# Kernel tuning notes

Hardware: AMD Instinct MI355X
Metric: run time of the kernel (lower is better)

Reference implementation:

```python
import jax, jax.numpy as jnp
import numpy as np
from jax import lax

# Config mirrors TemporalLePEAttention(dim=256, resolution=(56,56), idx=0, split_size=4, num_heads=8, temporal=True)
B, T, H, W, C = 2, 2, 56, 56, 256
NH = 8
HD = C // NH
SS = 4                      # split_size
H_sp, W_sp = H, SS          # idx == 0 -> strip windows of full height
nWh, nWw = H // H_sp, W // W_sp   # 1, 14
SCALE = HD ** -0.5
KH, KW = W_sp, H_sp         # unfold kernel = focal_window = [W_sp, H_sp] = (4, 56)
PH, PW = 0, H_sp // 2       # idx == 0 padding = [0, H_sp//2]
NW = B * nWh * nWw          # number of windows
TQ = T * H_sp * W_sp        # query tokens per window


def setup_inputs() -> dict:
    key = jax.random.key(0)
    k1, k2 = jax.random.split(key, 2)
    qkv = jax.random.normal(k1, (3, B, T, H, W, C), jnp.float32)
    # depthwise 3x3 LePE conv (nn.Conv2d(dim, dim, 3, padding=1, groups=dim))
    get_v_w = jax.random.normal(k2, (C, 1, 3, 3), jnp.float32) * 0.1
    get_v_b = jnp.zeros((C,), jnp.float32)
    # pool linear initialized as in the module: weight = SS/(H_sp*W_sp), bias = 0
    pool_w = jnp.full((SS, H_sp * W_sp), SS / (H_sp * W_sp), jnp.float32)
    pool_b = jnp.zeros((SS,), jnp.float32)
    return {"qkv": qkv, "get_v_w": get_v_w, "get_v_b": get_v_b,
            "pool_w": pool_w, "pool_b": pool_b}


def _windows_thw(x):
    # im2ddca_temporal: (B,T,H,W,C) -> (B*nWh*nWw, NH, T*H_sp*W_sp, HD)
    x = x.reshape(B, T, nWh, H_sp, nWw, W_sp, C).transpose(0, 2, 4, 1, 3, 5, 6)
    x = x.reshape(NW, TQ, NH, HD).transpose(0, 2, 1, 3)
    return x


def _lepe_temporal(v, w, b):
    # get_lepe_temporal: window v, depthwise 3x3 conv, return (v_win, lepe) as (NW, NH, TQ, HD)
    xw = v.reshape(B, T, nWh, H_sp, nWw, W_sp, C).transpose(0, 2, 4, 1, 6, 3, 5)
    xw = xw.reshape(-1, C, H_sp, W_sp)  # (B*nWh*nWw*T, C, H_sp, W_sp)
    lepe = lax.conv_general_dilated(xw, w, (1, 1), 'SAME', feature_group_count=C,
                                    dimension_numbers=('NCHW', 'OIHW', 'NCHW'))
    lepe = lepe + b[None, :, None, None]

    def fmt(t):
        t = t.reshape(NW, T, NH, HD, H_sp * W_sp).transpose(0, 2, 1, 4, 3)
        return t.reshape(NW, NH, TQ, HD)
    return fmt(xw), fmt(lepe)


def _pool_unfold(t, pool_w, pool_b):
    # focal pooling: per-window linear over H_sp*W_sp -> SS, then unfold over pooled map
    tw = t.reshape(B, T, nWh, H_sp, nWw, W_sp, C).transpose(0, 2, 4, 1, 6, 3, 5)
    tw = tw.reshape(B, nWh, nWw, T, C, H_sp * W_sp)
    p = jnp.einsum('bhwtcn,sn->bhwtcs', tw, pool_w) + pool_b  # (B,nWh,nWw,T,C,SS)
    # flatten(-2) + permute + reshape -> pooled map (B*T, C, SS*nWh, nWw)  (idx == 0)
    pm = p.transpose(0, 3, 4, 5, 1, 2).reshape(B * T, C, SS * nWh, nWw)
    # nn.Unfold(kernel=(KH,KW), padding=(PH,PW), stride=1); here out_h == 1
    pmp = jnp.pad(pm, ((0, 0), (0, 0), (PH, PH), (PW, PW)))
    ow = pmp.shape[3] - KW + 1  # = nWw + 1
    patches = jnp.stack([pmp[:, :, :, i:i + KW] for i in range(ow)], axis=1)  # (BT, ow, C, KH, KW)
    u = patches.reshape(B, T, ow, C, KH, KW).transpose(0, 2, 1, 4, 5, 3)      # (B, ow, T, KH, KW, C)
    u = u.reshape(B * ow, T * KH * KW, NH, HD).transpose(0, 2, 1, 3)          # (B*ow, NH, Tkk, HD)
    # idx == 0: view (B, nWh, -1, ...) and drop the last unfold location -> one per window
    u = u.reshape(B, nWh, ow // nWh, NH, T * KH * KW, HD)[:, :, :-1]
    return u.reshape(NW, NH, T * KH * KW, HD)


def reference(qkv, get_v_w, get_v_b, pool_w, pool_b):
    q_in, k_in, v_in = qkv[0], qkv[1], qkv[2]
    q = _windows_thw(q_in) * SCALE                      # (NW, NH, TQ, HD)
    k = _windows_thw(k_in)
    v, lepe = _lepe_temporal(v_in, get_v_w, get_v_b)
    kp = _pool_unfold(k_in, pool_w, pool_b)             # (NW, NH, TQ, HD)
    vp = _pool_unfold(v_in, pool_w, pool_b)
    k = jnp.concatenate([k, kp], axis=2)                # (NW, NH, 2*TQ, HD)
    v = jnp.concatenate([v, vp], axis=2)
    attn = jax.nn.softmax(jnp.einsum('wnqd,wnkd->wnqk', q, k), axis=-1)
    x = jnp.einsum('wnqk,wnkd->wnqd', attn, v) + lepe   # (NW, NH, TQ, HD)
    x = x.transpose(0, 2, 1, 3).reshape(NW, TQ, C)
    # windows2img_temporal -> (B, T, H, W, C)
    x = x.reshape(B, nWh, nWw, T, H_sp, W_sp, C).transpose(0, 3, 1, 4, 2, 5, 6)
    return x.reshape(B, T, H, W, C)
```

## Files before the change

### kernel.cpp

```cpp
#include <hip/hip_runtime.h>
#include <hip/hip_bf16.h>

#define B_   2
#define T_   2
#define H_   56
#define W_   56
#define C_   256
#define NH_  8
#define HD_  32
#define NWW_ 14
#define TQ_  448
#define SEQ_ 576
#define REAL_ 560
#define VIRT_ 320.0f
#define MEXP_ 16.0f
#define PMSTR_ 57344

typedef __bf16 bf16;
typedef __bf16 bf16x8 __attribute__((ext_vector_type(8)));
typedef __bf16 bf16x4 __attribute__((ext_vector_type(4)));
typedef float  f32x4  __attribute__((ext_vector_type(4)));
typedef short  s16x4  __attribute__((ext_vector_type(4)));
typedef unsigned int  uint;
typedef uint   uint4v __attribute__((ext_vector_type(4)));
typedef uint   uint2v __attribute__((ext_vector_type(2)));
typedef unsigned short u16;

#if defined(__has_builtin)
#  if __has_builtin(__builtin_amdgcn_mfma_f32_16x16x16bf16_1k)
#    define USE_MFMA16 1
#  endif
#endif
#ifndef USE_MFMA16
#  define USE_MFMA16 0
#endif

__device__ __forceinline__ uint pack2(float a, float b) {
    u16 ha = __builtin_bit_cast(u16, (bf16)a);
    u16 hb = __builtin_bit_cast(u16, (bf16)b);
    return (uint)ha | ((uint)hb << 16);
}

__global__ void pre_kernel(const float* __restrict__ k_in, const float* __restrict__ v_in,
                           const float* __restrict__ pool_w, const float* __restrict__ pool_b,
                           const float* __restrict__ gw, const float* __restrict__ gb,
                           float* __restrict__ pmk_part, float* __restrict__ pmv_part,
                           bf16* __restrict__ lepe) {
    __shared__ float pws[4][56];
    const int bid = blockIdx.x;
    const int c   = threadIdx.x;

    if (bid < 224) {
        const int quarter = bid & 3;
        const int bj = bid >> 2;
        const int j  = bj % NWW_;
        const int t  = (bj / NWW_) % T_;
        const int b  = bj / (NWW_ * T_);
        const int n0 = quarter * 56;

        if (c < 224) pws[c / 56][c % 56] = pool_w[(c / 56) * 224 + n0 + (c % 56)];
        __syncthreads();

        float ak[4], av[4];
        #pragma unroll
        for (int s = 0; s < 4; ++s) {
            ak[s] = (quarter == 0) ? pool_b[s] : 0.f;
            av[s] = 0.f;
        }
        for (int i = 0; i < 56; ++i) {
            const int n = n0 + i;
            const int h = n >> 2, wi = n & 3;
            const size_t off = ((size_t)(((b * T_ + t) * H_ + h) * W_ + (j * 4 + wi))) * C_ + c;
            const float kv = k_in[off];
            const float vv = v_in[off];
            #pragma unroll
            for (int s = 0; s < 4; ++s) {
                ak[s] += kv * pws[s][i];
                av[s] += vv * pws[s][i];
            }
        }
        #pragma unroll
        for (int s = 0; s < 4; ++s) {
            const size_t o = (size_t)quarter * PMSTR_ +
                             ((size_t)(((b * T_ + t) * 4 + s) * NWW_ + j)) * C_ + c;
            pmk_part[o] = ak[s];
            pmv_part[o] = av[s];
        }
    } else {
        const int r  = bid - 224;
        const int sp = r % 7;
        const int h  = (r / 7) % H_;
        const int bt = r / (7 * H_);

        float wv9[9];
        #pragma unroll
        for (int k = 0; k < 9; ++k) wv9[k] = gw[c * 9 + k];
        const float bias = gb[c];

        #pragma unroll
        for (int s2 = 0; s2 < 2; ++s2) {
            const int strip = sp * 2 + s2;
            float tile[3][4];
            #pragma unroll
            for (int dy = 0; dy < 3; ++dy) {
                const int hh = h - 1 + dy;
                const bool ok = (hh >= 0 && hh < H_);
                #pragma unroll
                for (int x = 0; x < 4; ++x) {
                    tile[dy][x] = ok
                        ? v_in[((size_t)(bt * H_ + hh) * W_ + (strip * 4 + x)) * C_ + c]
                        : 0.f;
                }
            }
            #pragma unroll
            for (int wi = 0; wi < 4; ++wi) {
                float acc = bias;
                #pragma unroll
                for (int dy = 0; dy < 3; ++dy) {
                    #pragma unroll
                    for (int dx = -1; dx <= 1; ++dx) {
                        const int xx = wi + dx;
                        if (xx >= 0 && xx < 4)
                            acc += wv9[dy * 3 + dx + 1] * tile[dy][xx];
                    }
                }
                lepe[((size_t)(bt * H_ + h) * W_ + (strip * 4 + wi)) * C_ + c] = (bf16)acc;
            }
        }
    }
}

__launch_bounds__(896, 4)
__global__ void attn_kernel(const float* __restrict__ q_in, const float* __restrict__ k_in,
                            const float* __restrict__ v_in, const float* __restrict__ pm_k,
                            const float* __restrict__ pm_v, const bf16* __restrict__ lepe,
                            float* __restrict__ out) {
    __shared__ __align__(16) u16 Ks[SEQ_ * 40];
    __shared__ __align__(16) u16 Vt[32 * 584];

    const int tid  = threadIdx.x;
    const int nh   = blockIdx.x & 7;
    const int nwi  = blockIdx.x >> 3;
    const int b    = nwi / NWW_;
    const int ww   = nwi % NWW_;
    const int cbase = nh * 32;

    for (int idx = tid; idx < SEQ_ * 4; idx += 896) {
        const int tok = idx >> 2, slot = idx & 3;
        uint4v dk = {0, 0, 0, 0}, dv = {0, 0, 0, 0};
        if (tok < TQ_) {
            const int t = tok / 224, r = tok % 224;
            const int h = r >> 2, wi = r & 3;
            const size_t off =
                ((size_t)(((b * T_ + t) * H_ + h) * W_ + (ww * 4 + wi))) * C_ + cbase + slot * 8;
            const f32x4 k0 = *(const f32x4*)(k_in + off);
            const f32x4 k1 = *(const f32x4*)(k_in + off + 4);
            const f32x4 v0 = *(const f32x4*)(v_in + off);
            const f32x4 v1 = *(const f32x4*)(v_in + off + 4);
            dk = uint4v{pack2(k0[0], k0[1]), pack2(k0[2], k0[3]),
                        pack2(k1[0], k1[1]), pack2(k1[2], k1[3])};
            dv = uint4v{pack2(v0[0], v0[1]), pack2(v0[2], v0[3]),
                        pack2(v1[0], v1[1]), pack2(v1[2], v1[3])};
        } else if (tok < REAL_) {
            const int i = tok - TQ_;
            const int t = i / 56, r = i % 56;
            const int kh = r / 14, jj = r % 14;
            const size_t off =
                ((size_t)(((b * T_ + t) * 4 + kh) * NWW_ + jj)) * C_ + cbase + slot * 8;
            f32x4 k0 = {0,0,0,0}, k1 = {0,0,0,0}, v0 = {0,0,0,0}, v1 = {0,0,0,0};
            #pragma unroll
            for (int pq = 0; pq < 4; ++pq) {
                const float* pk = pm_k + (size_t)pq * PMSTR_ + off;
                const float* pv = pm_v + (size_t)pq * PMSTR_ + off;
                k0 += *(const f32x4*)pk;  k1 += *(const f32x4*)(pk + 4);
                v0 += *(const f32x4*)pv;  v1 += *(const f32x4*)(pv + 4);
            }
            dk = uint4v{pack2(k0[0], k0[1]), pack2(k0[2], k0[3]),
                        pack2(k1[0], k1[1]), pack2(k1[2], k1[3])};
            dv = uint4v{pack2(v0[0], v0[1]), pack2(v0[2], v0[3]),
                        pack2(v1[0], v1[1]), pack2(v1[2], v1[3])};
        }
        *(uint4v*)(Ks + tok * 40 + slot * 8) = dk;
        u16 es[8];
        #pragma unroll
        for (int e = 0; e < 8; ++e) es[e] = (u16)((dv[e >> 1] >> ((e & 1) * 16)) & 0xffff);
        #pragma unroll
        for (int e = 0; e < 8; ++e) Vt[(slot * 8 + e) * 584 + tok] = es[e];
    }
    __syncthreads();

    const int lane = tid & 63;
    const int wv   = tid >> 6;
    const int l15  = lane & 15;
    const int g    = lane >> 4;
    const float QS = 0.17677669529663687f * 1.4426950408889634f;

    bf16x8 qf[2];
    #pragma unroll
    for (int ti = 0; ti < 2; ++ti) {
        const int qrow = (wv + ti * 14) * 16 + l15;
        const int t = qrow / 224, r = qrow % 224;
        const int h = r >> 2, wi = r & 3;
        const size_t off =
            ((size_t)(((b * T_ + t) * H_ + h) * W_ + (ww * 4 + wi))) * C_ + cbase + g * 8;
        const f32x4 a0 = *(const f32x4*)(q_in + off);
        const f32x4 a1 = *(const f32x4*)(q_in + off + 4);
        const uint4v qp = {pack2(a0[0] * QS, a0[1] * QS), pack2(a0[2] * QS, a0[3] * QS),
                           pack2(a1[0] * QS, a1[1] * QS), pack2(a1[2] * QS, a1[3] * QS)};
        qf[ti] = __builtin_bit_cast(bf16x8, qp);
    }

    f32x4 o[2][2];
    float ssum[2];
    const f32x4 zf = {0.f, 0.f, 0.f, 0.f};
    #pragma unroll
    for (int ti = 0; ti < 2; ++ti) {
        o[ti][0] = zf; o[ti][1] = zf; ssum[ti] = 0.f;
    }

    for (int kc = 0; kc < SEQ_ / 32; ++kc) {
        const int kt0 = kc * 32;
        const bf16x8 ka = *(const bf16x8*)(Ks + (kt0 + l15) * 40 + g * 8);
        const bf16x8 kb = *(const bf16x8*)(Ks + (kt0 + 16 + l15) * 40 + g * 8);
#if USE_MFMA16
        const s16x4 va00 = __builtin_bit_cast(s16x4, *(const uint2v*)(Vt + l15 * 584 + kt0 + g * 4));
        const s16x4 va01 = __builtin_bit_cast(s16x4, *(const uint2v*)(Vt + l15 * 584 + kt0 + 16 + g * 4));
        const s16x4 va10 = __builtin_bit_cast(s16x4, *(const uint2v*)(Vt + (16 + l15) * 584 + kt0 + g * 4));
        const s16x4 va11 = __builtin_bit_cast(s16x4, *(const uint2v*)(Vt + (16 + l15) * 584 + kt0 + 16 + g * 4));
#else
        const bf16x8 va = *(const bf16x8*)(Vt + l15 * 584 + kt0 + g * 8);
        const bf16x8 vb = *(const bf16x8*)(Vt + (16 + l15) * 584 + kt0 + g * 8);
#endif

        #pragma unroll
        for (int ti = 0; ti < 2; ++ti) {
            const f32x4 s0 = __builtin_amdgcn_mfma_f32_16x16x32_bf16(ka, qf[ti], zf, 0, 0, 0);
            const f32x4 s1 = __builtin_amdgcn_mfma_f32_16x16x32_bf16(kb, qf[ti], zf, 0, 0, 0);

            const float p0 = __builtin_amdgcn_exp2f(s0[0] - MEXP_);
            const float p1 = __builtin_amdgcn_exp2f(s0[1] - MEXP_);
            const float p2 = __builtin_amdgcn_exp2f(s0[2] - MEXP_);
            const float p3 = __builtin_amdgcn_exp2f(s0[3] - MEXP_);
            const float p4 = __builtin_amdgcn_exp2f(s1[0] - MEXP_);
            const float p5 = __builtin_amdgcn_exp2f(s1[1] - MEXP_);
            const float p6 = __builtin_amdgcn_exp2f(s1[2] - MEXP_);
            const float p7 = __builtin_amdgcn_exp2f(s1[3] - MEXP_);

            ssum[ti] += ((p0 + p1) + (p2 + p3)) + ((p4 + p5) + (p6 + p7));

            const uint w0 = pack2(p0, p1), w1 = pack2(p2, p3);
            const uint w2 = pack2(p4, p5), w3 = pack2(p6, p7);
#if USE_MFMA16
            const s16x4 pb0 = __builtin_bit_cast(s16x4, uint2v{w0, w1});
            const s16x4 pb1 = __builtin_bit_cast(s16x4, uint2v{w2, w3});
            o[ti][0] = __builtin_amdgcn_mfma_f32_16x16x16bf16_1k(va00, pb0, o[ti][0], 0, 0, 0);
            o[ti][0] = __builtin_amdgcn_mfma_f32_16x16x16bf16_1k(va01, pb1, o[ti][0], 0, 0, 0);
            o[ti][1] = __builtin_amdgcn_mfma_f32_16x16x16bf16_1k(va10, pb0, o[ti][1], 0, 0, 0);
            o[ti][1] = __builtin_amdgcn_mfma_f32_16x16x16bf16_1k(va11, pb1, o[ti][1], 0, 0, 0);
#else
            const int baseln = l15 + ((g & 1) << 5);
            const uint sA = (g & 2) ? w2 : w0;
            const uint sB = (g & 2) ? w3 : w1;
            const uint o0 = (uint)__shfl((int)sA, baseln);
            const uint o1 = (uint)__shfl((int)sB, baseln);
            const uint o2 = (uint)__shfl((int)sA, baseln + 16);
            const uint o3 = (uint)__shfl((int)sB, baseln + 16);
            const bf16x8 pf = __builtin_bit_cast(bf16x8, uint4v{o0, o1, o2, o3});
            o[ti][0] = __builtin_amdgcn_mfma_f32_16x16x32_bf16(pf, va, o[ti][0], 0, 0, 0);
            o[ti][1] = __builtin_amdgcn_mfma_f32_16x16x32_bf16(pf, vb, o[ti][1], 0, 0, 0);
#endif
        }
    }

    #pragma unroll
    for (int ti = 0; ti < 2; ++ti) {
        float den = ssum[ti];
        den += __shfl_xor(den, 16);
        den += __shfl_xor(den, 32);
        den += VIRT_ * 0.0000152587890625f;
        const float osc = 1.0f / den;

#if USE_MFMA16
        const int qrow = (wv + ti * 14) * 16 + l15;
        const int t = qrow / 224, rr = qrow % 224;
        const int h = rr >> 2, wi = rr & 3;
        const size_t off =
            ((size_t)(((b * T_ + t) * H_ + h) * W_ + (ww * 4 + wi))) * C_ + cbase;
        #pragma unroll
        for (int h2 = 0; h2 < 2; ++h2) {
            const int co = h2 * 16 + g * 4;
            const bf16x4 lp = *(const bf16x4*)(lepe + off + co);
            f32x4 val;
            #pragma unroll
            for (int r = 0; r < 4; ++r) val[r] = o[ti][h2][r] * osc + (float)lp[r];
            *(f32x4*)(out + off + co) = val;
        }
#else
        #pragma unroll
        for (int r = 0; r < 4; ++r) {
            const float oscr = __shfl(osc, g * 4 + r);
            const int qrow = (wv + ti * 14) * 16 + g * 4 + r;
            const int t = qrow / 224, rr = qrow % 224;
            const int h = rr >> 2, wi = rr & 3;
            const size_t off =
                ((size_t)(((b * T_ + t) * H_ + h) * W_ + (ww * 4 + wi))) * C_ + cbase + l15;
            out[off]      = o[ti][0][r] * oscr + (float)lepe[off];
            out[off + 16] = o[ti][1][r] * oscr + (float)lepe[off + 16];
        }
#endif
    }
}

extern "C" void kernel_launch(void* const* d_in, const int* in_sizes, int n_in,
                              void* d_out, int out_size, void* d_ws, size_t ws_size,
                              hipStream_t stream) {
    const float* qkv = (const float*)d_in[0];
    const float* gw  = (const float*)d_in[1];
    const float* gb  = (const float*)d_in[2];
    const float* pw  = (const float*)d_in[3];
    const float* pb  = (const float*)d_in[4];

    const size_t plane = (size_t)B_ * T_ * H_ * W_ * C_;
    const float* q_in = qkv;
    const float* k_in = qkv + plane;
    const float* v_in = qkv + 2 * plane;

    float* pmk_part = (float*)d_ws;
    float* pmv_part = pmk_part + 4 * PMSTR_;
    bf16*  lepe     = (bf16*)(pmv_part + 4 * PMSTR_);
    float* outp     = (float*)d_out;

    hipLaunchKernelGGL(pre_kernel, dim3(224 + 1568), dim3(256), 0, stream,
                       k_in, v_in, pw, pb, gw, gb, pmk_part, pmv_part, lepe);
    hipLaunchKernelGGL(attn_kernel, dim3(28 * 8), dim3(896), 0, stream,
                       q_in, k_in, v_in, pmk_part, pmv_part, lepe, outp);
}
```

Baseline: 44.51 us.

## Split attention blocks across query halves, pad K rows to 36, prefetch K/V fragments

```diff
diff --git a/kernel.cpp b/kernel.cpp
--- a/kernel.cpp
+++ b/kernel.cpp
@@ -15,6 +15,7 @@
 #define VIRT_ 320.0f
 #define MEXP_ 16.0f
 #define PMSTR_ 57344
+#define KSTR_ 36
 
 typedef __bf16 bf16;
 typedef __bf16 bf16x8 __attribute__((ext_vector_type(8)));
@@ -39,6 +40,13 @@
     u16 ha = __builtin_bit_cast(u16, (bf16)a);
     u16 hb = __builtin_bit_cast(u16, (bf16)b);
     return (uint)ha | ((uint)hb << 16);
+}
+
+__device__ __forceinline__ bf16x8 ldK(const u16* p) {
+    const uint2v a = *(const uint2v*)p;
+    const uint2v b = *(const uint2v*)(p + 4);
+    const uint4v u = {a[0], a[1], b[0], b[1]};
+    return __builtin_bit_cast(bf16x8, u);
 }
 
 __global__ void pre_kernel(const float* __restrict__ k_in, const float* __restrict__ v_in,
@@ -130,22 +138,24 @@
     }
 }
 
-__launch_bounds__(896, 4)
+__launch_bounds__(448, 4)
 __global__ void attn_kernel(const float* __restrict__ q_in, const float* __restrict__ k_in,
                             const float* __restrict__ v_in, const float* __restrict__ pm_k,
                             const float* __restrict__ pm_v, const bf16* __restrict__ lepe,
                             float* __restrict__ out) {
-    __shared__ __align__(16) u16 Ks[SEQ_ * 40];
+    __shared__ __align__(16) u16 Ks[SEQ_ * KSTR_];
     __shared__ __align__(16) u16 Vt[32 * 584];
 
     const int tid  = threadIdx.x;
-    const int nh   = blockIdx.x & 7;
-    const int nwi  = blockIdx.x >> 3;
+    const int bid  = blockIdx.x;
+    const int half = bid & 1;
+    const int nh   = (bid >> 1) & 7;
+    const int nwi  = bid >> 4;
     const int b    = nwi / NWW_;
     const int ww   = nwi % NWW_;
     const int cbase = nh * 32;
 
-    for (int idx = tid; idx < SEQ_ * 4; idx += 896) {
+    for (int idx = tid; idx < SEQ_ * 4; idx += 448) {
         const int tok = idx >> 2, slot = idx & 3;
         uint4v dk = {0, 0, 0, 0}, dv = {0, 0, 0, 0};
         if (tok < TQ_) {
@@ -180,7 +190,8 @@
             dv = uint4v{pack2(v0[0], v0[1]), pack2(v0[2], v0[3]),
                         pack2(v1[0], v1[1]), pack2(v1[2], v1[3])};
         }
-        *(uint4v*)(Ks + tok * 40 + slot * 8) = dk;
+        *(uint2v*)(Ks + tok * KSTR_ + slot * 8)     = uint2v{dk[0], dk[1]};
+        *(uint2v*)(Ks + tok * KSTR_ + slot * 8 + 4) = uint2v{dk[2], dk[3]};
         u16 es[8];
         #pragma unroll
         for (int e = 0; e < 8; ++e) es[e] = (u16)((dv[e >> 1] >> ((e & 1) * 16)) & 0xffff);
@@ -195,10 +206,11 @@
     const int g    = lane >> 4;
     const float QS = 0.17677669529663687f * 1.4426950408889634f;
 
+    const int tbase = half * 14 + wv;
     bf16x8 qf[2];
     #pragma unroll
     for (int ti = 0; ti < 2; ++ti) {
-        const int qrow = (wv + ti * 14) * 16 + l15;
+        const int qrow = (tbase + ti * 7) * 16 + l15;
         const int t = qrow / 224, r = qrow % 224;
         const int h = r >> 2, wi = r & 3;
         const size_t off =
@@ -218,24 +230,13 @@
         o[ti][0] = zf; o[ti][1] = zf; ssum[ti] = 0.f;
     }
 
-    for (int kc = 0; kc < SEQ_ / 32; ++kc) {
-        const int kt0 = kc * 32;
-        const bf16x8 ka = *(const bf16x8*)(Ks + (kt0 + l15) * 40 + g * 8);
-        const bf16x8 kb = *(const bf16x8*)(Ks + (kt0 + 16 + l15) * 40 + g * 8);
 #if USE_MFMA16
-        const s16x4 va00 = __builtin_bit_cast(s16x4, *(const uint2v*)(Vt + l15 * 584 + kt0 + g * 4));
-        const s16x4 va01 = __builtin_bit_cast(s16x4, *(const uint2v*)(Vt + l15 * 584 + kt0 + 16 + g * 4));
-        const s16x4 va10 = __builtin_bit_cast(s16x4, *(const uint2v*)(Vt + (16 + l15) * 584 + kt0 + g * 4));
-        const s16x4 va11 = __builtin_bit_cast(s16x4, *(const uint2v*)(Vt + (16 + l15) * 584 + kt0 + 16 + g * 4));
-#else
-        const bf16x8 va = *(const bf16x8*)(Vt + l15 * 584 + kt0 + g * 8);
-        const bf16x8 vb = *(const bf16x8*)(Vt + (16 + l15) * 584 + kt0 + g * 8);
-#endif
-
+    auto compute = [&](const bf16x8& KA, const bf16x8& KB, const s16x4& V00,
+                       const s16x4& V01, const s16x4& V10, const s16x4& V11) {
         #pragma unroll
         for (int ti = 0; ti < 2; ++ti) {
-            const f32x4 s0 = __builtin_amdgcn_mfma_f32_16x16x32_bf16(ka, qf[ti], zf, 0, 0, 0);
-            const f32x4 s1 = __builtin_amdgcn_mfma_f32_16x16x32_bf16(kb, qf[ti], zf, 0, 0, 0);
+            const f32x4 s0 = __builtin_amdgcn_mfma_f32_16x16x32_bf16(KA, qf[ti], zf, 0, 0, 0);
+            const f32x4 s1 = __builtin_amdgcn_mfma_f32_16x16x32_bf16(KB, qf[ti], zf, 0, 0, 0);
 
             const float p0 = __builtin_amdgcn_exp2f(s0[0] - MEXP_);
             const float p1 = __builtin_amdgcn_exp2f(s0[1] - MEXP_);
@@ -248,16 +249,63 @@
 
             ssum[ti] += ((p0 + p1) + (p2 + p3)) + ((p4 + p5) + (p6 + p7));
 
+            const s16x4 pb0 = __builtin_bit_cast(s16x4, uint2v{pack2(p0, p1), pack2(p2, p3)});
+            const s16x4 pb1 = __builtin_bit_cast(s16x4, uint2v{pack2(p4, p5), pack2(p6, p7)});
+            o[ti][0] = __builtin_amdgcn_mfma_f32_16x16x16bf16_1k(V00, pb0, o[ti][0], 0, 0, 0);
+            o[ti][0] = __builtin_amdgcn_mfma_f32_16x16x16bf16_1k(V01, pb1, o[ti][0], 0, 0, 0);
+            o[ti][1] = __builtin_amdgcn_mfma_f32_16x16x16bf16_1k(V10, pb0, o[ti][1], 0, 0, 0);
+            o[ti][1] = __builtin_amdgcn_mfma_f32_16x16x16bf16_1k(V11, pb1, o[ti][1], 0, 0, 0);
+        }
+    };
+
+    #define LOADF(KC, KA, KB, V00, V01, V10, V11) { \
+        const int kt_ = (KC) * 32; \
+        KA = ldK(Ks + (kt_ + l15) * KSTR_ + g * 8); \
+        KB = ldK(Ks + (kt_ + 16 + l15) * KSTR_ + g * 8); \
+        V00 = __builtin_bit_cast(s16x4, *(const uint2v*)(Vt + l15 * 584 + kt_ + g * 4)); \
+        V01 = __builtin_bit_cast(s16x4, *(const uint2v*)(Vt + l15 * 584 + kt_ + 16 + g * 4)); \
+        V10 = __builtin_bit_cast(s16x4, *(const uint2v*)(Vt + (16 + l15) * 584 + kt_ + g * 4)); \
+        V11 = __builtin_bit_cast(s16x4, *(const uint2v*)(Vt + (16 + l15) * 584 + kt_ + 16 + g * 4)); }
+
+    bf16x8 kaC, kbC;
+    s16x4 vC00, vC01, vC10, vC11;
+    LOADF(0, kaC, kbC, vC00, vC01, vC10, vC11);
+    for (int kc = 0; kc < SEQ_ / 32 - 1; ++kc) {
+        bf16x8 kaN, kbN;
+        s16x4 vN00, vN01, vN10, vN11;
+        LOADF(kc + 1, kaN, kbN, vN00, vN01, vN10, vN11);
+        compute(kaC, kbC, vC00, vC01, vC10, vC11);
+        kaC = kaN; kbC = kbN;
+        vC00 = vN00; vC01 = vN01; vC10 = vN10; vC11 = vN11;
+    }
+    compute(kaC, kbC, vC00, vC01, vC10, vC11);
+    #undef LOADF
+#else
+    for (int kc = 0; kc < SEQ_ / 32; ++kc) {
+        const int kt0 = kc * 32;
+        const bf16x8 ka = ldK(Ks + (kt0 + l15) * KSTR_ + g * 8);
+        const bf16x8 kb = ldK(Ks + (kt0 + 16 + l15) * KSTR_ + g * 8);
+        const bf16x8 va = *(const bf16x8*)(Vt + l15 * 584 + kt0 + g * 8);
+        const bf16x8 vb = *(const bf16x8*)(Vt + (16 + l15) * 584 + kt0 + g * 8);
+
+        #pragma unroll
+        for (int ti = 0; ti < 2; ++ti) {
+            const f32x4 s0 = __builtin_amdgcn_mfma_f32_16x16x32_bf16(ka, qf[ti], zf, 0, 0, 0);
+            const f32x4 s1 = __builtin_amdgcn_mfma_f32_16x16x32_bf16(kb, qf[ti], zf, 0, 0, 0);
+
+            const float p0 = __builtin_amdgcn_exp2f(s0[0] - MEXP_);
+            const float p1 = __builtin_amdgcn_exp2f(s0[1] - MEXP_);
+            const float p2 = __builtin_amdgcn_exp2f(s0[2] - MEXP_);
+            const float p3 = __builtin_amdgcn_exp2f(s0[3] - MEXP_);
+            const float p4 = __builtin_amdgcn_exp2f(s1[0] - MEXP_);
+            const float p5 = __builtin_amdgcn_exp2f(s1[1] - MEXP_);
+            const float p6 = __builtin_amdgcn_exp2f(s1[2] - MEXP_);
+            const float p7 = __builtin_amdgcn_exp2f(s1[3] - MEXP_);
+
+            ssum[ti] += ((p0 + p1) + (p2 + p3)) + ((p4 + p5) + (p6 + p7));
+
             const uint w0 = pack2(p0, p1), w1 = pack2(p2, p3);
             const uint w2 = pack2(p4, p5), w3 = pack2(p6, p7);
-#if USE_MFMA16
-            const s16x4 pb0 = __builtin_bit_cast(s16x4, uint2v{w0, w1});
-            const s16x4 pb1 = __builtin_bit_cast(s16x4, uint2v{w2, w3});
-            o[ti][0] = __builtin_amdgcn_mfma_f32_16x16x16bf16_1k(va00, pb0, o[ti][0], 0, 0, 0);
-            o[ti][0] = __builtin_amdgcn_mfma_f32_16x16x16bf16_1k(va01, pb1, o[ti][0], 0, 0, 0);
-            o[ti][1] = __builtin_amdgcn_mfma_f32_16x16x16bf16_1k(va10, pb0, o[ti][1], 0, 0, 0);
-            o[ti][1] = __builtin_amdgcn_mfma_f32_16x16x16bf16_1k(va11, pb1, o[ti][1], 0, 0, 0);
-#else
             const int baseln = l15 + ((g & 1) << 5);
             const uint sA = (g & 2) ? w2 : w0;
             const uint sB = (g & 2) ? w3 : w1;
@@ -268,9 +316,9 @@
             const bf16x8 pf = __builtin_bit_cast(bf16x8, uint4v{o0, o1, o2, o3});
             o[ti][0] = __builtin_amdgcn_mfma_f32_16x16x32_bf16(pf, va, o[ti][0], 0, 0, 0);
             o[ti][1] = __builtin_amdgcn_mfma_f32_16x16x32_bf16(pf, vb, o[ti][1], 0, 0, 0);
+        }
+    }
 #endif
-        }
-    }
 
     #pragma unroll
     for (int ti = 0; ti < 2; ++ti) {
@@ -281,7 +329,7 @@
         const float osc = 1.0f / den;
 
 #if USE_MFMA16
-        const int qrow = (wv + ti * 14) * 16 + l15;
+        const int qrow = (tbase + ti * 7) * 16 + l15;
         const int t = qrow / 224, rr = qrow % 224;
         const int h = rr >> 2, wi = rr & 3;
         const size_t off =
@@ -299,7 +347,7 @@
         #pragma unroll
         for (int r = 0; r < 4; ++r) {
             const float oscr = __shfl(osc, g * 4 + r);
-            const int qrow = (wv + ti * 14) * 16 + g * 4 + r;
+            const int qrow = (tbase + ti * 7) * 16 + g * 4 + r;
             const int t = qrow / 224, rr = qrow % 224;
             const int h = rr >> 2, wi = rr & 3;
             const size_t off =
@@ -332,6 +380,6 @@
 
     hipLaunchKernelGGL(pre_kernel, dim3(224 + 1568), dim3(256), 0, stream,
                        k_in, v_in, pw, pb, gw, gb, pmk_part, pmv_part, lepe);
-    hipLaunchKernelGGL(attn_kernel, dim3(28 * 8), dim3(896), 0, stream,
+    hipLaunchKernelGGL(attn_kernel, dim3(28 * 8 * 2), dim3(448), 0, stream,
                        q_in, k_in, v_in, pmk_part, pmv_part, lepe, outp);
 }
```

New measurement: 46.34 us. +4.1%, slower.

## Drop LDS staging in attention; each wave streams K/V from global

Applied to the files above, without the earlier changes.

```diff
diff --git a/kernel.cpp b/kernel.cpp
--- a/kernel.cpp
+++ b/kernel.cpp
@@ -9,12 +9,11 @@
 #define NH_  8
 #define HD_  32
 #define NWW_ 14
+#define WC_  (W_ * C_)
+#define P1_  (H_ * W_ * C_)
 #define TQ_  448
-#define SEQ_ 576
-#define REAL_ 560
-#define VIRT_ 320.0f
+#define VIRT_ 336.0f
 #define MEXP_ 16.0f
-#define PMSTR_ 57344
 
 typedef __bf16 bf16;
 typedef __bf16 bf16x8 __attribute__((ext_vector_type(8)));
@@ -26,71 +25,88 @@
 typedef uint   uint2v __attribute__((ext_vector_type(2)));
 typedef unsigned short u16;
 
-#if defined(__has_builtin)
-#  if __has_builtin(__builtin_amdgcn_mfma_f32_16x16x16bf16_1k)
-#    define USE_MFMA16 1
-#  endif
-#endif
-#ifndef USE_MFMA16
-#  define USE_MFMA16 0
-#endif
-
 __device__ __forceinline__ uint pack2(float a, float b) {
     u16 ha = __builtin_bit_cast(u16, (bf16)a);
     u16 hb = __builtin_bit_cast(u16, (bf16)b);
     return (uint)ha | ((uint)hb << 16);
 }
 
+__device__ __forceinline__ bf16x8 pack8(const float* __restrict__ p) {
+    const f32x4 a = *(const f32x4*)p;
+    const f32x4 b = *(const f32x4*)(p + 4);
+    const uint4v u = {pack2(a[0], a[1]), pack2(a[2], a[3]),
+                      pack2(b[0], b[1]), pack2(b[2], b[3])};
+    return __builtin_bit_cast(bf16x8, u);
+}
+
+__device__ __forceinline__ s16x4 pack4(float a, float b, float c, float d) {
+    const uint2v u = {pack2(a, b), pack2(c, d)};
+    return __builtin_bit_cast(s16x4, u);
+}
+
+__launch_bounds__(1024, 1)
 __global__ void pre_kernel(const float* __restrict__ k_in, const float* __restrict__ v_in,
                            const float* __restrict__ pool_w, const float* __restrict__ pool_b,
                            const float* __restrict__ gw, const float* __restrict__ gb,
-                           float* __restrict__ pmk_part, float* __restrict__ pmv_part,
+                           float* __restrict__ pm_k, float* __restrict__ pm_v,
                            bf16* __restrict__ lepe) {
-    __shared__ float pws[4][56];
     const int bid = blockIdx.x;
-    const int c   = threadIdx.x;
-
-    if (bid < 224) {
-        const int quarter = bid & 3;
-        const int bj = bid >> 2;
-        const int j  = bj % NWW_;
-        const int t  = (bj / NWW_) % T_;
-        const int b  = bj / (NWW_ * T_);
+    const int tid = threadIdx.x;
+
+    if (bid < 56) {
+        __shared__ float pws[4][224];
+        __shared__ float red[3][4][2][256];
+        const int j = bid % NWW_;
+        const int t = (bid / NWW_) % T_;
+        const int b = bid / (NWW_ * T_);
+        const int quarter = tid >> 8;
+        const int c = tid & 255;
+
+        if (tid < 896) pws[tid / 224][tid % 224] = pool_w[tid];
+        __syncthreads();
+
+        float ak[4] = {0.f, 0.f, 0.f, 0.f};
+        float av[4] = {0.f, 0.f, 0.f, 0.f};
         const int n0 = quarter * 56;
-
-        if (c < 224) pws[c / 56][c % 56] = pool_w[(c / 56) * 224 + n0 + (c % 56)];
-        __syncthreads();
-
-        float ak[4], av[4];
-        #pragma unroll
-        for (int s = 0; s < 4; ++s) {
-            ak[s] = (quarter == 0) ? pool_b[s] : 0.f;
-            av[s] = 0.f;
-        }
+        #pragma unroll 4
         for (int i = 0; i < 56; ++i) {
             const int n = n0 + i;
             const int h = n >> 2, wi = n & 3;
-            const size_t off = ((size_t)(((b * T_ + t) * H_ + h) * W_ + (j * 4 + wi))) * C_ + c;
+            const size_t off = (size_t)(b * T_ + t) * P1_ + h * WC_ + (j * 4 + wi) * C_ + c;
             const float kv = k_in[off];
             const float vv = v_in[off];
             #pragma unroll
             for (int s = 0; s < 4; ++s) {
-                ak[s] += kv * pws[s][i];
-                av[s] += vv * pws[s][i];
-            }
-        }
-        #pragma unroll
-        for (int s = 0; s < 4; ++s) {
-            const size_t o = (size_t)quarter * PMSTR_ +
-                             ((size_t)(((b * T_ + t) * 4 + s) * NWW_ + j)) * C_ + c;
-            pmk_part[o] = ak[s];
-            pmv_part[o] = av[s];
+                ak[s] += kv * pws[s][n];
+                av[s] += vv * pws[s][n];
+            }
+        }
+        if (quarter > 0) {
+            #pragma unroll
+            for (int s = 0; s < 4; ++s) {
+                red[quarter - 1][s][0][c] = ak[s];
+                red[quarter - 1][s][1][c] = av[s];
+            }
+        }
+        __syncthreads();
+        if (quarter == 0) {
+            #pragma unroll
+            for (int s = 0; s < 4; ++s) {
+                const float bias = pool_b[s];
+                const float sk = ak[s] + red[0][s][0][c] + red[1][s][0][c] + red[2][s][0][c] + bias;
+                const float sv = av[s] + red[0][s][1][c] + red[1][s][1][c] + red[2][s][1][c] + bias;
+                const size_t o = ((size_t)(((b * T_ + t) * 4 + s) * NWW_ + j)) * C_ + c;
+                pm_k[o] = sk;
+                pm_v[o] = sv;
+            }
         }
     } else {
-        const int r  = bid - 224;
+        const int r  = bid - 56;
         const int sp = r % 7;
-        const int h  = (r / 7) % H_;
-        const int bt = r / (7 * H_);
+        const int hq = (r / 7) % NWW_;
+        const int bt = r / (7 * NWW_);
+        const int h  = hq * 4 + (tid >> 8);
+        const int c  = tid & 255;
 
         float wv9[9];
         #pragma unroll
@@ -108,7 +124,7 @@
                 #pragma unroll
                 for (int x = 0; x < 4; ++x) {
                     tile[dy][x] = ok
-                        ? v_in[((size_t)(bt * H_ + hh) * W_ + (strip * 4 + x)) * C_ + c]
+                        ? v_in[(size_t)bt * P1_ + hh * WC_ + (strip * 4 + x) * C_ + c]
                         : 0.f;
                 }
             }
@@ -124,85 +140,38 @@
                             acc += wv9[dy * 3 + dx + 1] * tile[dy][xx];
                     }
                 }
-                lepe[((size_t)(bt * H_ + h) * W_ + (strip * 4 + wi)) * C_ + c] = (bf16)acc;
-            }
-        }
-    }
-}
-
-__launch_bounds__(896, 4)
+                lepe[(size_t)bt * P1_ + h * WC_ + (strip * 4 + wi) * C_ + c] = (bf16)acc;
+            }
+        }
+    }
+}
+
+__launch_bounds__(256, 4)
 __global__ void attn_kernel(const float* __restrict__ q_in, const float* __restrict__ k_in,
                             const float* __restrict__ v_in, const float* __restrict__ pm_k,
                             const float* __restrict__ pm_v, const bf16* __restrict__ lepe,
                             float* __restrict__ out) {
-    __shared__ __align__(16) u16 Ks[SEQ_ * 40];
-    __shared__ __align__(16) u16 Vt[32 * 584];
-
     const int tid  = threadIdx.x;
-    const int nh   = blockIdx.x & 7;
-    const int nwi  = blockIdx.x >> 3;
+    const int lane = tid & 63;
+    const int wvid = (blockIdx.x << 2) + (tid >> 6);
+    const int wpair = wvid % 14;
+    const int hw   = wvid / 14;
+    const int nh   = hw & 7;
+    const int nwi  = hw >> 3;
     const int b    = nwi / NWW_;
     const int ww   = nwi % NWW_;
-    const int cbase = nh * 32;
-
-    for (int idx = tid; idx < SEQ_ * 4; idx += 896) {
-        const int tok = idx >> 2, slot = idx & 3;
-        uint4v dk = {0, 0, 0, 0}, dv = {0, 0, 0, 0};
-        if (tok < TQ_) {
-            const int t = tok / 224, r = tok % 224;
-            const int h = r >> 2, wi = r & 3;
-            const size_t off =
-                ((size_t)(((b * T_ + t) * H_ + h) * W_ + (ww * 4 + wi))) * C_ + cbase + slot * 8;
-            const f32x4 k0 = *(const f32x4*)(k_in + off);
-            const f32x4 k1 = *(const f32x4*)(k_in + off + 4);
-            const f32x4 v0 = *(const f32x4*)(v_in + off);
-            const f32x4 v1 = *(const f32x4*)(v_in + off + 4);
-            dk = uint4v{pack2(k0[0], k0[1]), pack2(k0[2], k0[3]),
-                        pack2(k1[0], k1[1]), pack2(k1[2], k1[3])};
-            dv = uint4v{pack2(v0[0], v0[1]), pack2(v0[2], v0[3]),
-                        pack2(v1[0], v1[1]), pack2(v1[2], v1[3])};
-        } else if (tok < REAL_) {
-            const int i = tok - TQ_;
-            const int t = i / 56, r = i % 56;
-            const int kh = r / 14, jj = r % 14;
-            const size_t off =
-                ((size_t)(((b * T_ + t) * 4 + kh) * NWW_ + jj)) * C_ + cbase + slot * 8;
-            f32x4 k0 = {0,0,0,0}, k1 = {0,0,0,0}, v0 = {0,0,0,0}, v1 = {0,0,0,0};
-            #pragma unroll
-            for (int pq = 0; pq < 4; ++pq) {
-                const float* pk = pm_k + (size_t)pq * PMSTR_ + off;
-                const float* pv = pm_v + (size_t)pq * PMSTR_ + off;
-                k0 += *(const f32x4*)pk;  k1 += *(const f32x4*)(pk + 4);
-                v0 += *(const f32x4*)pv;  v1 += *(const f32x4*)(pv + 4);
-            }
-            dk = uint4v{pack2(k0[0], k0[1]), pack2(k0[2], k0[3]),
-                        pack2(k1[0], k1[1]), pack2(k1[2], k1[3])};
-            dv = uint4v{pack2(v0[0], v0[1]), pack2(v0[2], v0[3]),
-                        pack2(v1[0], v1[1]), pack2(v1[2], v1[3])};
-        }
-        *(uint4v*)(Ks + tok * 40 + slot * 8) = dk;
-        u16 es[8];
-        #pragma unroll
-        for (int e = 0; e < 8; ++e) es[e] = (u16)((dv[e >> 1] >> ((e & 1) * 16)) & 0xffff);
-        #pragma unroll
-        for (int e = 0; e < 8; ++e) Vt[(slot * 8 + e) * 584 + tok] = es[e];
-    }
-    __syncthreads();
-
-    const int lane = tid & 63;
-    const int wv   = tid >> 6;
     const int l15  = lane & 15;
     const int g    = lane >> 4;
+    const int cbase = nh * 32;
     const float QS = 0.17677669529663687f * 1.4426950408889634f;
 
     bf16x8 qf[2];
     #pragma unroll
     for (int ti = 0; ti < 2; ++ti) {
-        const int qrow = (wv + ti * 14) * 16 + l15;
+        const int qrow = (wpair + ti * 14) * 16 + l15;
         const int t = qrow / 224, r = qrow % 224;
         const int h = r >> 2, wi = r & 3;
-        const size_t off =
-            ((size_t)(((b * T_ + t) * H_ + h) * W_ + (ww * 4 + wi))) * C_ + cbase + g * 8;
+        const size_t off = (size_t)(b * T_ + t) * P1_ + h * WC_ + (ww * 4 + wi) * C_ + cbase + g * 8;
         const f32x4 a0 = *(const f32x4*)(q_in + off);
         const f32x4 a1 = *(const f32x4*)(q_in + off + 4);
         const uint4v qp = {pack2(a0[0] * QS, a0[1] * QS), pack2(a0[2] * QS, a0[3] * QS),
@@ -214,29 +183,14 @@
     float ssum[2];
     const f32x4 zf = {0.f, 0.f, 0.f, 0.f};
     #pragma unroll
-    for (int ti = 0; ti < 2; ++ti) {
-        o[ti][0] = zf; o[ti][1] = zf; ssum[ti] = 0.f;
-    }
-
-    for (int kc = 0; kc < SEQ_ / 32; ++kc) {
-        const int kt0 = kc * 32;
-        const bf16x8 ka = *(const bf16x8*)(Ks + (kt0 + l15) * 40 + g * 8);
-        const bf16x8 kb = *(const bf16x8*)(Ks + (kt0 + 16 + l15) * 40 + g * 8);
-#if USE_MFMA16
-        const s16x4 va00 = __builtin_bit_cast(s16x4, *(const uint2v*)(Vt + l15 * 584 + kt0 + g * 4));
-        const s16x4 va01 = __builtin_bit_cast(s16x4, *(const uint2v*)(Vt + l15 * 584 + kt0 + 16 + g * 4));
-        const s16x4 va10 = __builtin_bit_cast(s16x4, *(const uint2v*)(Vt + (16 + l15) * 584 + kt0 + g * 4));
-        const s16x4 va11 = __builtin_bit_cast(s16x4, *(const uint2v*)(Vt + (16 + l15) * 584 + kt0 + 16 + g * 4));
-#else
-        const bf16x8 va = *(const bf16x8*)(Vt + l15 * 584 + kt0 + g * 8);
-        const bf16x8 vb = *(const bf16x8*)(Vt + (16 + l15) * 584 + kt0 + g * 8);
-#endif
-
+    for (int ti = 0; ti < 2; ++ti) { o[ti][0] = zf; o[ti][1] = zf; ssum[ti] = 0.f; }
+
+    auto computeFull = [&](const bf16x8& KA, const bf16x8& KB, const s16x4& V00,
+                           const s16x4& V01, const s16x4& V10, const s16x4& V11) {
         #pragma unroll
         for (int ti = 0; ti < 2; ++ti) {
-            const f32x4 s0 = __builtin_amdgcn_mfma_f32_16x16x32_bf16(ka, qf[ti], zf, 0, 0, 0);
-            const f32x4 s1 = __builtin_amdgcn_mfma_f32_16x16x32_bf16(kb, qf[ti], zf, 0, 0, 0);
-
+            const f32x4 s0 = __builtin_amdgcn_mfma_f32_16x16x32_bf16(KA, qf[ti], zf, 0, 0, 0);
+            const f32x4 s1 = __builtin_amdgcn_mfma_f32_16x16x32_bf16(KB, qf[ti], zf, 0, 0, 0);
             const float p0 = __builtin_amdgcn_exp2f(s0[0] - MEXP_);
             const float p1 = __builtin_amdgcn_exp2f(s0[1] - MEXP_);
             const float p2 = __builtin_amdgcn_exp2f(s0[2] - MEXP_);
@@ -245,30 +199,93 @@
             const float p5 = __builtin_amdgcn_exp2f(s1[1] - MEXP_);
             const float p6 = __builtin_amdgcn_exp2f(s1[2] - MEXP_);
             const float p7 = __builtin_amdgcn_exp2f(s1[3] - MEXP_);
-
             ssum[ti] += ((p0 + p1) + (p2 + p3)) + ((p4 + p5) + (p6 + p7));
-
-            const uint w0 = pack2(p0, p1), w1 = pack2(p2, p3);
-            const uint w2 = pack2(p4, p5), w3 = pack2(p6, p7);
-#if USE_MFMA16
-            const s16x4 pb0 = __builtin_bit_cast(s16x4, uint2v{w0, w1});
-            const s16x4 pb1 = __builtin_bit_cast(s16x4, uint2v{w2, w3});
-            o[ti][0] = __builtin_amdgcn_mfma_f32_16x16x16bf16_1k(va00, pb0, o[ti][0], 0, 0, 0);
-            o[ti][0] = __builtin_amdgcn_mfma_f32_16x16x16bf16_1k(va01, pb1, o[ti][0], 0, 0, 0);
-            o[ti][1] = __builtin_amdgcn_mfma_f32_16x16x16bf16_1k(va10, pb0, o[ti][1], 0, 0, 0);
-            o[ti][1] = __builtin_amdgcn_mfma_f32_16x16x16bf16_1k(va11, pb1, o[ti][1], 0, 0, 0);
-#else
-            const int baseln = l15 + ((g & 1) << 5);
-            const uint sA = (g & 2) ? w2 : w0;
-            const uint sB = (g & 2) ? w3 : w1;
-            const uint o0 = (uint)__shfl((int)sA, baseln);
-            const uint o1 = (uint)__shfl((int)sB, baseln);
-            const uint o2 = (uint)__shfl((int)sA, baseln + 16);
-            const uint o3 = (uint)__shfl((int)sB, baseln + 16);
-            const bf16x8 pf = __builtin_bit_cast(bf16x8, uint4v{o0, o1, o2, o3});
-            o[ti][0] = __builtin_amdgcn_mfma_f32_16x16x32_bf16(pf, va, o[ti][0], 0, 0, 0);
-            o[ti][1] = __builtin_amdgcn_mfma_f32_16x16x32_bf16(pf, vb, o[ti][1], 0, 0, 0);
-#endif
+            const s16x4 pb0 = pack4(p0, p1, p2, p3);
+            const s16x4 pb1 = pack4(p4, p5, p6, p7);
+            o[ti][0] = __builtin_amdgcn_mfma_f32_16x16x16bf16_1k(V00, pb0, o[ti][0], 0, 0, 0);
+            o[ti][0] = __builtin_amdgcn_mfma_f32_16x16x16bf16_1k(V01, pb1, o[ti][0], 0, 0, 0);
+            o[ti][1] = __builtin_amdgcn_mfma_f32_16x16x16bf16_1k(V10, pb0, o[ti][1], 0, 0, 0);
+            o[ti][1] = __builtin_amdgcn_mfma_f32_16x16x16bf16_1k(V11, pb1, o[ti][1], 0, 0, 0);
+        }
+    };
+    auto computeHalf = [&](const bf16x8& KA, const s16x4& V00, const s16x4& V10) {
+        #pragma unroll
+        for (int ti = 0; ti < 2; ++ti) {
+            const f32x4 s0 = __builtin_amdgcn_mfma_f32_16x16x32_bf16(KA, qf[ti], zf, 0, 0, 0);
+            const float p0 = __builtin_amdgcn_exp2f(s0[0] - MEXP_);
+            const float p1 = __builtin_amdgcn_exp2f(s0[1] - MEXP_);
+            const float p2 = __builtin_amdgcn_exp2f(s0[2] - MEXP_);
+            const float p3 = __builtin_amdgcn_exp2f(s0[3] - MEXP_);
+            ssum[ti] += (p0 + p1) + (p2 + p3);
+            const s16x4 pb0 = pack4(p0, p1, p2, p3);
+            o[ti][0] = __builtin_amdgcn_mfma_f32_16x16x16bf16_1k(V00, pb0, o[ti][0], 0, 0, 0);
+            o[ti][1] = __builtin_amdgcn_mfma_f32_16x16x16bf16_1k(V10, pb0, o[ti][1], 0, 0, 0);
+        }
+    };
+
+    const int koffA = (l15 >> 2) * WC_ + (l15 & 3) * C_ + cbase + g * 8;
+    const int voffA = g * WC_ + cbase + l15;
+
+    for (int t = 0; t < 2; ++t) {
+        const float* kb_ = k_in + (size_t)(b * T_ + t) * P1_ + ww * 4 * C_;
+        const float* vb_ = v_in + (size_t)(b * T_ + t) * P1_ + ww * 4 * C_;
+        #pragma unroll 1
+        for (int rc = 0; rc < 7; ++rc) {
+            const int cb = rc * 8 * WC_;
+            const bf16x8 ka = pack8(kb_ + cb + koffA);
+            const bf16x8 kb2 = pack8(kb_ + cb + koffA + 4 * WC_);
+            const float* vp = vb_ + cb + voffA;
+            const s16x4 v00 = pack4(vp[0], vp[C_], vp[2 * C_], vp[3 * C_]);
+            const s16x4 v01 = pack4(vp[4 * WC_], vp[4 * WC_ + C_],
+                                    vp[4 * WC_ + 2 * C_], vp[4 * WC_ + 3 * C_]);
+            const s16x4 v10 = pack4(vp[16], vp[C_ + 16], vp[2 * C_ + 16], vp[3 * C_ + 16]);
+            const s16x4 v11 = pack4(vp[4 * WC_ + 16], vp[4 * WC_ + C_ + 16],
+                                    vp[4 * WC_ + 2 * C_ + 16], vp[4 * WC_ + 3 * C_ + 16]);
+            computeFull(ka, kb2, v00, v01, v10, v11);
+        }
+    }
+
+    #pragma unroll 1
+    for (int pc = 0; pc < 4; ++pc) {
+        const int i0 = pc * 32 + l15;
+        const int t0 = i0 / 56, r0 = i0 - 56 * t0;
+        const int sx0 = r0 / 14, j0 = r0 - 14 * sx0;
+        const bf16x8 ka = pack8(pm_k + (size_t)(((b * T_ + t0) * 4 + sx0) * NWW_ + j0) * C_
+                                     + cbase + g * 8);
+        float f0[4], fh0[4];
+        #pragma unroll
+        for (int e = 0; e < 4; ++e) {
+            const int iv = pc * 32 + g * 4 + e;
+            const int tv = iv / 56, rv = iv - 56 * tv;
+            const int sv = rv / 14, jv = rv - 14 * sv;
+            const float* pv = pm_v + (size_t)(((b * T_ + tv) * 4 + sv) * NWW_ + jv) * C_
+                                   + cbase + l15;
+            f0[e] = pv[0]; fh0[e] = pv[16];
+        }
+        const s16x4 v00 = pack4(f0[0], f0[1], f0[2], f0[3]);
+        const s16x4 v10 = pack4(fh0[0], fh0[1], fh0[2], fh0[3]);
+
+        if (pc < 3) {
+            const int i1 = i0 + 16;
+            const int t1 = i1 / 56, r1 = i1 - 56 * t1;
+            const int sx1 = r1 / 14, j1 = r1 - 14 * sx1;
+            const bf16x8 kb2 = pack8(pm_k + (size_t)(((b * T_ + t1) * 4 + sx1) * NWW_ + j1) * C_
+                                          + cbase + g * 8);
+            float f1[4], fh1[4];
+            #pragma unroll
+            for (int e = 0; e < 4; ++e) {
+                const int iv = pc * 32 + 16 + g * 4 + e;
+                const int tv = iv / 56, rv = iv - 56 * tv;
+                const int sv = rv / 14, jv = rv - 14 * sv;
+                const float* pv = pm_v + (size_t)(((b * T_ + tv) * 4 + sv) * NWW_ + jv) * C_
+                                       + cbase + l15;
+                f1[e] = pv[0]; fh1[e] = pv[16];
+            }
+            const s16x4 v01 = pack4(f1[0], f1[1], f1[2], f1[3]);
+            const s16x4 v11 = pack4(fh1[0], fh1[1], fh1[2], fh1[3]);
+            computeFull(ka, kb2, v00, v01, v10, v11);
+        } else {
+            computeHalf(ka, v00, v10);
         }
     }
 
@@ -280,12 +297,10 @@
         den += VIRT_ * 0.0000152587890625f;
         const float osc = 1.0f / den;
 
-#if USE_MFMA16
-        const int qrow = (wv + ti * 14) * 16 + l15;
+        const int qrow = (wpair + ti * 14) * 16 + l15;
         const int t = qrow / 224, rr = qrow % 224;
         const int h = rr >> 2, wi = rr & 3;
-        const size_t off =
-            ((size_t)(((b * T_ + t) * H_ + h) * W_ + (ww * 4 + wi))) * C_ + cbase;
+        const size_t off = (size_t)(b * T_ + t) * P1_ + h * WC_ + (ww * 4 + wi) * C_ + cbase;
         #pragma unroll
         for (int h2 = 0; h2 < 2; ++h2) {
             const int co = h2 * 16 + g * 4;
@@ -295,19 +310,6 @@
             for (int r = 0; r < 4; ++r) val[r] = o[ti][h2][r] * osc + (float)lp[r];
             *(f32x4*)(out + off + co) = val;
         }
-#else
-        #pragma unroll
-        for (int r = 0; r < 4; ++r) {
-            const float oscr = __shfl(osc, g * 4 + r);
-            const int qrow = (wv + ti * 14) * 16 + g * 4 + r;
-            const int t = qrow / 224, rr = qrow % 224;
-            const int h = rr >> 2, wi = rr & 3;
-            const size_t off =
-                ((size_t)(((b * T_ + t) * H_ + h) * W_ + (ww * 4 + wi))) * C_ + cbase + l15;
-            out[off]      = o[ti][0][r] * oscr + (float)lepe[off];
-            out[off + 16] = o[ti][1][r] * oscr + (float)lepe[off + 16];
-        }
-#endif
     }
 }
 
@@ -325,13 +327,14 @@
     const float* k_in = qkv + plane;
     const float* v_in = qkv + 2 * plane;
 
-    float* pmk_part = (float*)d_ws;
-    float* pmv_part = pmk_part + 4 * PMSTR_;
-    bf16*  lepe     = (bf16*)(pmv_part + 4 * PMSTR_);
-    float* outp     = (float*)d_out;
-
-    hipLaunchKernelGGL(pre_kernel, dim3(224 + 1568), dim3(256), 0, stream,
-                       k_in, v_in, pw, pb, gw, gb, pmk_part, pmv_part, lepe);
-    hipLaunchKernelGGL(attn_kernel, dim3(28 * 8), dim3(896), 0, stream,
-                       q_in, k_in, v_in, pmk_part, pmv_part, lepe, outp);
-}
+    const size_t pm_elems = (size_t)B_ * T_ * 4 * NWW_ * C_;
+    float* pm_k = (float*)d_ws;
+    float* pm_v = pm_k + pm_elems;
+    bf16*  lepe = (bf16*)(pm_v + pm_elems);
+    float* outp = (float*)d_out;
+
+    hipLaunchKernelGGL(pre_kernel, dim3(56 + 392), dim3(1024), 0, stream,
+                       k_in, v_in, pw, pb, gw, gb, pm_k, pm_v, lepe);
+    hipLaunchKernelGGL(attn_kernel, dim3(784), dim3(256), 0, stream,
+                       q_in, k_in, v_in, pm_k, pm_v, lepe, outp);
+}
```

New measurement: 64.04 us. 43.9% more time.
